# Performance work log

Hardware: AMD Instinct MI355X
Metric: run time of the kernel (lower is better)

## Reference

```python
import jax, jax.numpy as jnp
import numpy as np

L = 16384   # sequence length
H = 1024    # feature dim
P = 1024    # state dim (ssm_size=2048, conj_sym=True -> P = ssm_size//2)
STEP_RESCALE = 1.0
CLIP_MAX = -1e-4


def setup_inputs() -> dict:
    key = jax.random.key(0)
    ks = jax.random.split(key, 7)
    log_dt_min, log_dt_max = np.log(0.001), np.log(0.1)
    return {
        "input_sequence": jax.random.normal(ks[0], (L, H), jnp.float32),
        # stable eigenvalues: negative real part
        "Lambda_re": -(jnp.abs(jax.random.normal(ks[1], (P,), jnp.float32)) + 1e-3),
        "Lambda_im": jax.random.normal(ks[2], (P,), jnp.float32) * jnp.pi,
        "B": jax.random.normal(ks[3], (P, H, 2), jnp.float32) / np.sqrt(H),
        "C": jax.random.normal(ks[4], (H, P, 2), jnp.float32) / np.sqrt(P),
        "D": jax.random.normal(ks[5], (H,), jnp.float32),
        "log_step": jax.random.uniform(ks[6], (P, 1), jnp.float32,
                                        minval=log_dt_min, maxval=log_dt_max),
    }


def _binop(q_i, q_j):
    # binary operator of the linear recurrence (diagonal A)
    A_i, b_i = q_i
    A_j, b_j = q_j
    return (A_j * A_i, A_j * b_i + b_j)


def reference(input_sequence, Lambda_re, Lambda_im, B, C, D, log_step):
    # clip_eigs=True: clamp real part at -1e-4
    Lambda = jnp.minimum(Lambda_re, CLIP_MAX) + 1j * Lambda_im        # (P,) complex64
    B_tilde = B[..., 0] + 1j * B[..., 1]                              # (P, H)
    C_tilde = C[..., 0] + 1j * C[..., 1]                              # (H, P)
    step = STEP_RESCALE * jnp.exp(log_step[:, 0])                     # (P,)
    # ZOH discretisation
    Lambda_bar = jnp.exp(Lambda * step)                               # (P,)
    B_bar = ((Lambda_bar - 1.0) / Lambda)[:, None] * B_tilde          # (P, H)
    # input projection: (L,H) @ (H,P) -> (L,P) complex
    Bu = input_sequence.astype(B_bar.dtype) @ B_bar.T
    Lam = jnp.broadcast_to(Lambda_bar, Bu.shape)                      # (L, P)
    # parallel (Blelchley-style) associative scan over time
    _, xs = jax.lax.associative_scan(_binop, (Lam, Bu))               # (L, P)
    # output projection; conj_sym=True -> factor 2 on the real part
    ys = 2.0 * jnp.real(xs @ C_tilde.T)                               # (L, H)
    return ys + input_sequence * D
```

## Files before the change

### kernel.cpp

```cpp
#include <hip/hip_runtime.h>
#include <hip/hip_bf16.h>
#include <stdint.h>


#define L_SEQ 16384
#define H_DIM 1024
#define P_DIM 1024
#define NCH   256
#define TCH   64

typedef __bf16 bf16x8 __attribute__((ext_vector_type(8)));
typedef float  floatx4 __attribute__((ext_vector_type(4)));
using bf16 = __hip_bfloat16;

__device__ __forceinline__ void gld_lds16(const void* g, void* l) {
    __builtin_amdgcn_global_load_lds(
        (const __attribute__((address_space(1))) uint32_t*)g,
        (__attribute__((address_space(3))) uint32_t*)l, 16, 0, 0);
}

__device__ __forceinline__ float lo_bf(uint32_t v) { return __uint_as_float(v << 16); }
__device__ __forceinline__ float hi_bf(uint32_t v) { return __uint_as_float(v & 0xffff0000u); }
__device__ __forceinline__ uint32_t pack_bf(float r, float i) {
    bf16 rb = __float2bfloat16(r), ib = __float2bfloat16(i);
    return ((uint32_t)(*(uint16_t*)&ib) << 16) | (uint32_t)(*(uint16_t*)&rb);
}

__device__ __forceinline__ float rd(const void* p, size_t i, int f) {
    return f ? ((const float*)p)[i]
             : __bfloat162float(((const bf16*)p)[i]);
}

__device__ __forceinline__ int detect_f32(const uint16_t* u) {
    __shared__ int cnt;
    if (threadIdx.x == 0) cnt = 0;
    __syncthreads();
    int c = 0;
    #pragma unroll
    for (int i = 0; i < 8; ++i) {
        int e = (u[threadIdx.x * 8 + i] >> 7) & 0xFF;
        c += (e >= 134);
    }
    if (c) atomicAdd(&cnt, c);
    __syncthreads();
    return cnt > 32;
}

__global__ void convert_u(const void* __restrict__ uin, bf16* __restrict__ ub) {
    const int f = detect_f32((const uint16_t*)uin);
    const size_t g = (size_t)blockIdx.x * 256 + threadIdx.x;
    if (f) {
        const float4* s = (const float4*)uin + g * 2;
        float4 a = s[0], b = s[1];
        alignas(16) bf16 t[8] = {
            __float2bfloat16(a.x), __float2bfloat16(a.y),
            __float2bfloat16(a.z), __float2bfloat16(a.w),
            __float2bfloat16(b.x), __float2bfloat16(b.y),
            __float2bfloat16(b.z), __float2bfloat16(b.w)};
        ((uint4*)ub)[g] = *(const uint4*)t;
    } else {
        ((uint4*)ub)[g] = ((const uint4*)uin)[g];
    }
}

__global__ void prep_all(const void* __restrict__ u,
                         const void* __restrict__ Lre, const void* __restrict__ Lim,
                         const void* __restrict__ lstep, const void* __restrict__ B,
                         const void* __restrict__ C, const void* __restrict__ D,
                         bf16* __restrict__ W1t, bf16* __restrict__ W2t,
                         float* __restrict__ d_f,
                         float2* __restrict__ lam, float2* __restrict__ lamT) {
    const int f = detect_f32((const uint16_t*)u);
    const int p = blockIdx.x;
    float lr = fminf(rd(Lre, p, f), -1e-4f);
    float li = rd(Lim, p, f);
    float s  = expf(rd(lstep, p, f));
    float ea = expf(lr * s);
    float lbr = ea * cosf(li * s), lbi = ea * sinf(li * s);
    float dr = lbr - 1.0f, di = lbi;
    float den = lr * lr + li * li;
    float cr = (dr * lr + di * li) / den;
    float ci = (di * lr - dr * li) / den;
    if (threadIdx.x == 0) {
        lam[p] = make_float2(lbr, lbi);
        float tr = lbr, ti = lbi;
        #pragma unroll
        for (int q = 0; q < 6; ++q) {
            float nr = tr * tr - ti * ti, ni = 2.0f * tr * ti;
            tr = nr; ti = ni;
        }
        lamT[p] = make_float2(tr, ti);
        d_f[p] = rd(D, p, f);
    }
    for (int h = threadIdx.x; h < H_DIM; h += blockDim.x) {
        size_t base = ((size_t)p * H_DIM + h) * 2;
        float br = rd(B, base + 0, f);
        float bi = rd(B, base + 1, f);
        W1t[(size_t)(2 * p)     * H_DIM + h] = __float2bfloat16(cr * br - ci * bi);
        W1t[(size_t)(2 * p + 1) * H_DIM + h] = __float2bfloat16(cr * bi + ci * br);
    }
    const int h = blockIdx.x;
    for (int q = threadIdx.x; q < P_DIM; q += blockDim.x) {
        size_t base = ((size_t)h * P_DIM + q) * 2;
        W2t[(size_t)h * (2 * P_DIM) + 2 * q]     = __float2bfloat16( 2.0f * rd(C, base + 0, f));
        W2t[(size_t)h * (2 * P_DIM) + 2 * q + 1] = __float2bfloat16(-2.0f * rd(C, base + 1, f));
    }
}

template <int N, int K, bool EPI>
__global__ __launch_bounds__(256) void gemm_bt(
    const bf16* __restrict__ A, const bf16* __restrict__ Bt,
    bf16* __restrict__ OutBF, float* __restrict__ OutF,
    const bf16* __restrict__ U, const float* __restrict__ Dvec) {
    constexpr int NXB = N / 128;
    __shared__ alignas(16) uint8_t sA[128 * 128];
    __shared__ alignas(16) uint8_t sB[128 * 128];

    const int tid  = threadIdx.x;
    const int wave = tid >> 6;
    const int lane = tid & 63;
    const int bid = blockIdx.x;
    const int xr  = bid & 7;
    const int jj  = bid >> 3;
    const int bx  = jj % NXB;
    const int by  = (jj / NXB) * 8 + xr;
    const int bm  = by * 128, bn = bx * 128;
    const int wm  = (wave >> 1) * 64, wn = (wave & 1) * 64;

    floatx4 acc[4][4] = {};

    const int fr   = lane & 15;
    const int kq   = lane >> 4;
    const int srow = tid >> 3;
    const int skc  = tid & 7;

    for (int k0 = 0; k0 < K; k0 += 64) {
        #pragma unroll
        for (int q = 0; q < 4; ++q) {
            const int row = q * 32 + srow;
            const int kcg = skc ^ (row & 7);
            gld_lds16(A  + (size_t)(bm + row) * K + k0 + kcg * 8,
                      sA + q * 4096 + wave * 1024);
            gld_lds16(Bt + (size_t)(bn + row) * K + k0 + kcg * 8,
                      sB + q * 4096 + wave * 1024);
        }
        __syncthreads();
        #pragma unroll
        for (int s = 0; s < 2; ++s) {
            bf16x8 af[4], bfr[4];
            #pragma unroll
            for (int mi = 0; mi < 4; ++mi) {
                const int row = wm + mi * 16 + fr;
                const int ch  = (s * 4 + kq) ^ (row & 7);
                af[mi] = *(const bf16x8*)(sA + row * 128 + ch * 16);
            }
            #pragma unroll
            for (int ni = 0; ni < 4; ++ni) {
                const int row = wn + ni * 16 + fr;
                const int ch  = (s * 4 + kq) ^ (row & 7);
                bfr[ni] = *(const bf16x8*)(sB + row * 128 + ch * 16);
            }
            #pragma unroll
            for (int mi = 0; mi < 4; ++mi)
                #pragma unroll
                for (int ni = 0; ni < 4; ++ni)
                    acc[mi][ni] = __builtin_amdgcn_mfma_f32_16x16x32_bf16(
                        af[mi], bfr[ni], acc[mi][ni], 0, 0, 0);
        }
        __syncthreads();
    }

    const int col0  = bn + wn + fr;
    const int rbase = bm + wm + kq * 4;
    #pragma unroll
    for (int mi = 0; mi < 4; ++mi) {
        #pragma unroll
        for (int rr = 0; rr < 4; ++rr) {
            const int row = rbase + mi * 16 + rr;
            #pragma unroll
            for (int ni = 0; ni < 4; ++ni) {
                const int c = col0 + ni * 16;
                float v = acc[mi][ni][rr];
                if (EPI) {
                    float uu = __bfloat162float(U[(size_t)row * H_DIM + c]);
                    __builtin_nontemporal_store(v + uu * Dvec[c],
                                                &OutF[(size_t)row * N + c]);
                } else {
                    OutBF[(size_t)row * N + c] = __float2bfloat16(v);
                }
            }
        }
    }
}

__global__ void scan_phase1(const uint32_t* __restrict__ Bu,
                            const float2* __restrict__ lam,
                            float2* __restrict__ agg) {
    const int p = blockIdx.y * 256 + threadIdx.x;
    const int c = blockIdx.x;
    const float2 lb = lam[p];
    float xr = 0.f, xi = 0.f;
    const uint32_t* b = Bu + (size_t)c * TCH * P_DIM + p;
    #pragma unroll 4
    for (int j = 0; j < TCH; ++j) {
        uint32_t v = *b;
        float nr = lb.x * xr - lb.y * xi + lo_bf(v);
        float ni = lb.x * xi + lb.y * xr + hi_bf(v);
        xr = nr; xi = ni;
        b += P_DIM;
    }
    agg[(size_t)c * P_DIM + p] = make_float2(xr, xi);
}

__global__ void scan_phase2(const float2* __restrict__ agg,
                            const float2* __restrict__ lamT,
                            float2* __restrict__ carry) {
    const int p = blockIdx.x * 256 + threadIdx.x;
    const float2 lT = lamT[p];
    float cr = 0.f, ci = 0.f;
    #pragma unroll 4
    for (int c = 0; c < NCH; ++c) {
        carry[(size_t)c * P_DIM + p] = make_float2(cr, ci);
        float2 a = agg[(size_t)c * P_DIM + p];
        float nr = lT.x * cr - lT.y * ci + a.x;
        float ni = lT.x * ci + lT.y * cr + a.y;
        cr = nr; ci = ni;
    }
}

__global__ void scan_phase3(uint32_t* __restrict__ BuX,
                            const float2* __restrict__ lam,
                            const float2* __restrict__ carry) {
    const int p = blockIdx.y * 256 + threadIdx.x;
    const int c = blockIdx.x;
    const float2 lb = lam[p];
    const float2 c0 = carry[(size_t)c * P_DIM + p];
    float xr = c0.x, xi = c0.y;
    uint32_t* b = BuX + (size_t)c * TCH * P_DIM + p;
    #pragma unroll 4
    for (int j = 0; j < TCH; ++j) {
        uint32_t v = *b;
        float nr = lb.x * xr - lb.y * xi + lo_bf(v);
        float ni = lb.x * xi + lb.y * xr + hi_bf(v);
        xr = nr; xi = ni;
        *b = pack_bf(xr, xi);
        b += P_DIM;
    }
}

extern "C" void kernel_launch(void* const* d_in, const int* in_sizes, int n_in,
                              void* d_out, int out_size, void* d_ws, size_t ws_size,
                              hipStream_t stream) {
    float* out = (float*)d_out;

    char* w = (char*)d_ws;
    w += 256;
    float2* lam   = (float2*)w;  w += (size_t)P_DIM * 8;
    float2* lamT  = (float2*)w;  w += (size_t)P_DIM * 8;
    float*  d_f   = (float*)w;   w += (size_t)H_DIM * 4;
    float2* agg   = (float2*)w;  w += (size_t)NCH * P_DIM * 8;
    float2* carry = (float2*)w;  w += (size_t)NCH * P_DIM * 8;
    bf16*   W1t   = (bf16*)w;    w += (size_t)2 * P_DIM * H_DIM * 2;
    bf16*   W2t   = (bf16*)w;    w += (size_t)H_DIM * 2 * P_DIM * 2;
    bf16*   ub    = (bf16*)w;    w += (size_t)L_SEQ * H_DIM * 2;
    bf16*   Xbuf  = (bf16*)w;

    convert_u<<<(L_SEQ * H_DIM / 8) / 256, 256, 0, stream>>>(d_in[0], ub);
    prep_all<<<P_DIM, 256, 0, stream>>>(d_in[0], d_in[1], d_in[2], d_in[6],
                                        d_in[3], d_in[4], d_in[5],
                                        W1t, W2t, d_f, lam, lamT);

    gemm_bt<2 * P_DIM, H_DIM, false><<<(2 * P_DIM / 128) * 128, 256, 0, stream>>>(
        ub, W1t, Xbuf, nullptr, nullptr, nullptr);

    scan_phase1<<<dim3(NCH, P_DIM / 256), 256, 0, stream>>>(
        (const uint32_t*)Xbuf, lam, agg);
    scan_phase2<<<P_DIM / 256, 256, 0, stream>>>(agg, lamT, carry);
    scan_phase3<<<dim3(NCH, P_DIM / 256), 256, 0, stream>>>(
        (uint32_t*)Xbuf, lam, carry);

    gemm_bt<H_DIM, 2 * P_DIM, true><<<(H_DIM / 128) * 128, 256, 0, stream>>>(
        Xbuf, W2t, nullptr, out, ub, d_f);
}
```

Before: 373.4 us.

## Fuse chunk-aggregate scan phase into input GEMM epilogue and parallelise carry scan

```diff
diff --git a/kernel.cpp b/kernel.cpp
--- a/kernel.cpp
+++ b/kernel.cpp
@@ -107,14 +107,16 @@
     }
 }
 
-template <int N, int K, bool EPI>
+template <int N, int K, int MODE>
 __global__ __launch_bounds__(256) void gemm_bt(
     const bf16* __restrict__ A, const bf16* __restrict__ Bt,
     bf16* __restrict__ OutBF, float* __restrict__ OutF,
-    const bf16* __restrict__ U, const float* __restrict__ Dvec) {
+    const bf16* __restrict__ U, const float* __restrict__ Dvec,
+    const float2* __restrict__ lam, float2* __restrict__ aggp) {
     constexpr int NXB = N / 128;
-    __shared__ alignas(16) uint8_t sA[128 * 128];
-    __shared__ alignas(16) uint8_t sB[128 * 128];
+    __shared__ alignas(16) uint8_t smem[32768];
+    uint8_t* sA = smem;
+    uint8_t* sB = smem + 16384;
 
     const int tid  = threadIdx.x;
     const int wave = tid >> 6;
@@ -181,7 +183,7 @@
             for (int ni = 0; ni < 4; ++ni) {
                 const int c = col0 + ni * 16;
                 float v = acc[mi][ni][rr];
-                if (EPI) {
+                if (MODE == 2) {
                     float uu = __bfloat162float(U[(size_t)row * H_DIM + c]);
                     __builtin_nontemporal_store(v + uu * Dvec[c],
                                                 &OutF[(size_t)row * N + c]);
@@ -191,40 +193,99 @@
             }
         }
     }
-}
-
-__global__ void scan_phase1(const uint32_t* __restrict__ Bu,
-                            const float2* __restrict__ lam,
-                            float2* __restrict__ agg) {
-    const int p = blockIdx.y * 256 + threadIdx.x;
-    const int c = blockIdx.x;
-    const float2 lb = lam[p];
+
+    if (MODE == 1) {
+        float2* wtab = (float2*)smem;
+        {
+            const int ql = tid >> 2;
+            const int t0 = (tid & 3) * 16;
+            float2 lb = lam[(bn >> 1) + ql];
+            float tr = lb.x, ti = lb.y;
+            #pragma unroll
+            for (int q = 0; q < 4; ++q) {
+                float nr = tr * tr - ti * ti, ni = 2.f * tr * ti;
+                tr = nr; ti = ni;
+            }
+            float p32r = tr * tr - ti * ti, p32i = 2.f * tr * ti;
+            float wr, wi;
+            if (t0 == 0)       { wr = p32r * tr - p32i * ti; wi = p32r * ti + p32i * tr; }
+            else if (t0 == 16) { wr = p32r; wi = p32i; }
+            else if (t0 == 32) { wr = tr;   wi = ti; }
+            else               { wr = 1.f;  wi = 0.f; }
+            #pragma unroll
+            for (int j = 15; j >= 0; --j) {
+                wtab[ql * 64 + t0 + j] = make_float2(wr, wi);
+                float nr = wr * lb.x - wi * lb.y;
+                float ni = wr * lb.y + wi * lb.x;
+                wr = nr; wi = ni;
+            }
+        }
+        __syncthreads();
+        const int par = fr & 1;
+        const int cg  = (bm + wm) >> 6;
+        #pragma unroll
+        for (int ni = 0; ni < 4; ++ni) {
+            const int ql = (wn + ni * 16 + (fr & ~1)) >> 1;
+            float s = 0.f;
+            #pragma unroll
+            for (int mi = 0; mi < 4; ++mi)
+                #pragma unroll
+                for (int rr = 0; rr < 4; ++rr) {
+                    const int t = mi * 16 + kq * 4 + rr;
+                    float own  = acc[mi][ni][rr];
+                    float part = __shfl_xor(own, 1);
+                    float2 wv = wtab[ql * 64 + t];
+                    s += wv.x * own + (par ? wv.y : -wv.y) * part;
+                }
+            s += __shfl_xor(s, 16);
+            s += __shfl_xor(s, 32);
+            float other = __shfl_xor(s, 1);
+            if (kq == 0 && par == 0)
+                aggp[(size_t)cg * P_DIM + (bn >> 1) + ql] = make_float2(s, other);
+        }
+    }
+}
+
+__global__ void scan_phase2p(const float2* __restrict__ agg,
+                             const float2* __restrict__ lamT,
+                             float2* __restrict__ carry) {
+    const int w = threadIdx.x >> 6;
+    const int j = threadIdx.x & 63;
+    const int p = blockIdx.x * 4 + w;
+    const float2 A = lamT[p];
+    float b2r = A.x * A.x - A.y * A.y, b2i = 2.f * A.x * A.y;
+    float Br = b2r * b2r - b2i * b2i, Bi = 2.f * b2r * b2i;
+    float2 a[4];
+    #pragma unroll
+    for (int k = 0; k < 4; ++k) a[k] = agg[(size_t)(4 * j + k) * P_DIM + p];
     float xr = 0.f, xi = 0.f;
-    const uint32_t* b = Bu + (size_t)c * TCH * P_DIM + p;
-    #pragma unroll 4
-    for (int j = 0; j < TCH; ++j) {
-        uint32_t v = *b;
-        float nr = lb.x * xr - lb.y * xi + lo_bf(v);
-        float ni = lb.x * xi + lb.y * xr + hi_bf(v);
+    #pragma unroll
+    for (int k = 0; k < 4; ++k) {
+        float nr = A.x * xr - A.y * xi + a[k].x;
+        float ni = A.x * xi + A.y * xr + a[k].y;
         xr = nr; xi = ni;
-        b += P_DIM;
-    }
-    agg[(size_t)c * P_DIM + p] = make_float2(xr, xi);
-}
-
-__global__ void scan_phase2(const float2* __restrict__ agg,
-                            const float2* __restrict__ lamT,
-                            float2* __restrict__ carry) {
-    const int p = blockIdx.x * 256 + threadIdx.x;
-    const float2 lT = lamT[p];
-    float cr = 0.f, ci = 0.f;
-    #pragma unroll 4
-    for (int c = 0; c < NCH; ++c) {
-        carry[(size_t)c * P_DIM + p] = make_float2(cr, ci);
-        float2 a = agg[(size_t)c * P_DIM + p];
-        float nr = lT.x * cr - lT.y * ci + a.x;
-        float ni = lT.x * ci + lT.y * cr + a.y;
-        cr = nr; ci = ni;
+    }
+    float cr = Br, ci = Bi, vr = xr, vi = xi;
+    #pragma unroll
+    for (int d = 1; d < 64; d <<= 1) {
+        float pvr = __shfl_up(vr, d), pvi = __shfl_up(vi, d);
+        float pcr = __shfl_up(cr, d), pci = __shfl_up(ci, d);
+        if (j >= d) {
+            float nvr = cr * pvr - ci * pvi + vr;
+            float nvi = cr * pvi + ci * pvr + vi;
+            float ncr = cr * pcr - ci * pci;
+            float nci = cr * pci + ci * pcr;
+            vr = nvr; vi = nvi; cr = ncr; ci = nci;
+        }
+    }
+    float sr = __shfl_up(vr, 1), si = __shfl_up(vi, 1);
+    if (j == 0) { sr = 0.f; si = 0.f; }
+    #pragma unroll
+    for (int k = 0; k < 4; ++k) {
+        carry[(size_t)(4 * j + k) * P_DIM + p] = make_float2(sr, si);
+        float nr = A.x * sr - A.y * si + a[k].x;
+        float ni = A.x * si + A.y * sr + a[k].y;
+        sr = nr; si = ni;
     }
 }
 
@@ -270,15 +331,13 @@
                                         d_in[3], d_in[4], d_in[5],
                                         W1t, W2t, d_f, lam, lamT);
 
-    gemm_bt<2 * P_DIM, H_DIM, false><<<(2 * P_DIM / 128) * 128, 256, 0, stream>>>(
-        ub, W1t, Xbuf, nullptr, nullptr, nullptr);
-
-    scan_phase1<<<dim3(NCH, P_DIM / 256), 256, 0, stream>>>(
-        (const uint32_t*)Xbuf, lam, agg);
-    scan_phase2<<<P_DIM / 256, 256, 0, stream>>>(agg, lamT, carry);
+    gemm_bt<2 * P_DIM, H_DIM, 1><<<(2 * P_DIM / 128) * 128, 256, 0, stream>>>(
+        ub, W1t, Xbuf, nullptr, nullptr, nullptr, lam, agg);
+
+    scan_phase2p<<<P_DIM / 4, 256, 0, stream>>>(agg, lamT, carry);
     scan_phase3<<<dim3(NCH, P_DIM / 256), 256, 0, stream>>>(
         (uint32_t*)Xbuf, lam, carry);
 
-    gemm_bt<H_DIM, 2 * P_DIM, true><<<(H_DIM / 128) * 128, 256, 0, stream>>>(
-        Xbuf, W2t, nullptr, out, ub, d_f);
-}
+    gemm_bt<H_DIM, 2 * P_DIM, 2><<<(H_DIM / 128) * 128, 256, 0, stream>>>(
+        Xbuf, W2t, nullptr, out, ub, d_f, nullptr, nullptr);
+}
```

Measured after the change: 361.9 us. 3.1% less time.
